# Performance work log

Hardware: AMD Instinct MI355X
Metric: run time of the kernel (lower is better)

## Reference

```python
import jax, jax.numpy as jnp
import numpy as np

B, D, H = 4096, 66, 512  # batch, system dim (22 atoms * 3), MLP hidden


def _dynamics(t, xs, W1, b1, W2, b2, W3, b3):
    # CNF vector field f(t, x): 3-layer SiLU MLP on concat([x, t])
    h = jnp.concatenate([xs, t], axis=1)          # [B, D+1]
    h = jax.nn.silu(h @ W1 + b1)                  # [B, H]
    h = jax.nn.silu(h @ W2 + b2)                  # [B, H]
    return h @ W3 + b3                            # [B, D]


def setup_inputs() -> dict:
    key = jax.random.key(0)
    ks = jax.random.split(key, 5)
    xs = jax.random.normal(ks[0], (B, D), dtype=jnp.float32)
    t = jax.random.uniform(ks[1], (B, 1), dtype=jnp.float32)
    W1 = jax.random.normal(ks[2], (D + 1, H), dtype=jnp.float32) / np.float32(np.sqrt(D + 1))
    b1 = jnp.zeros((H,), dtype=jnp.float32)
    W2 = jax.random.normal(ks[3], (H, H), dtype=jnp.float32) / np.float32(np.sqrt(H))
    b2 = jnp.zeros((H,), dtype=jnp.float32)
    W3 = jax.random.normal(ks[4], (H, D), dtype=jnp.float32) / np.float32(np.sqrt(H))
    b3 = jnp.zeros((D,), dtype=jnp.float32)
    return {"xs": xs, "t": t, "W1": W1, "b1": b1, "W2": W2, "b2": b2, "W3": W3, "b3": b3}


def reference(xs, t, W1, b1, W2, b2, W3, b3):
    # Exact divergence: trace of Jacobian d f / d x, computed with D JVPs
    # (forward-mode equivalent of the torch per-dim autograd.grad loop).
    def f(x):
        return _dynamics(t, x, W1, b1, W2, b2, W3, b3)

    dxs = f(xs)                                   # [B, D]
    eye = jnp.eye(D, dtype=xs.dtype)              # basis vectors e_i

    def jvp_col(e):
        _, tang = jax.jvp(f, (xs,), (jnp.broadcast_to(e, xs.shape),))
        return tang                               # J @ e_i, shape [B, D]

    tangs = jax.vmap(jvp_col)(eye)                # [D, B, D]
    div = jnp.einsum('dbd->b', tangs)             # sum_i (J e_i)_i = tr(J)
    return dxs, -div[:, None]
```

## Files before the change

### kernel.cpp

```cpp
#include <hip/hip_runtime.h>

#define Bn 4096
#define Dn 66
#define Hn 512

typedef __attribute__((ext_vector_type(8))) short short8;
typedef __attribute__((ext_vector_type(4))) float f32x4;

__device__ __forceinline__ unsigned short f2bf(float x) {
    union { float f; unsigned u; } v; v.f = x;
    unsigned r = v.u + 0x7fffu + ((v.u >> 16) & 1u);
    return (unsigned short)(r >> 16);
}
__device__ __forceinline__ float bf2f(unsigned short h) {
    union { float f; unsigned u; } v; v.u = ((unsigned)h) << 16; return v.f;
}


__global__ __launch_bounds__(512, 2) void k_pack(
    const float* __restrict__ W1, const float* __restrict__ W2,
    const float* __restrict__ W3,
    unsigned short* __restrict__ W2P, unsigned short* __restrict__ CmP,
    unsigned short* __restrict__ W3P)
{
    __shared__ float sW3[16*68];
    const int bid = blockIdx.x, tid = threadIdx.x;
    const int lane = tid & 63, wv = tid >> 6;

    if (bid < 64) {
        const int ct = bid >> 1;
        {
            const int r = tid >> 5, ii = tid & 31;
            const float* src = &W3[(size_t)(ct*16 + r)*Dn];
            sW3[r*68 + ii] = src[ii];
            sW3[r*68 + ii + 32] = src[ii + 32];
            if (ii < 2) sW3[r*68 + ii + 64] = src[ii + 64];
        }
        __syncthreads();
        const int ks = (bid & 1)*8 + wv;
        const int n = lane & 15, kg = lane >> 4;
        const int c = ct*16 + n;
        const int abase = ks*32 + kg*8;
        float w2v[8], m[8];
        #pragma unroll
        for (int j = 0; j < 8; ++j) {
            w2v[j] = W2[(size_t)(abase + j)*Hn + c];
            m[j] = 0.f;
        }
        #pragma unroll 2
        for (int i = 0; i < Dn; ++i) {
            const float w3 = sW3[n*68 + i];
            const float4 w1a = *(const float4*)&W1[(size_t)i*Hn + abase];
            const float4 w1b = *(const float4*)&W1[(size_t)i*Hn + abase + 4];
            m[0] = fmaf(w3, w1a.x, m[0]); m[1] = fmaf(w3, w1a.y, m[1]);
            m[2] = fmaf(w3, w1a.z, m[2]); m[3] = fmaf(w3, w1a.w, m[3]);
            m[4] = fmaf(w3, w1b.x, m[4]); m[5] = fmaf(w3, w1b.y, m[5]);
            m[6] = fmaf(w3, w1b.z, m[6]); m[7] = fmaf(w3, w1b.w, m[7]);
        }
        short8 pw, pc;
        #pragma unroll
        for (int j = 0; j < 8; ++j) {
            pw[j] = (short)f2bf(w2v[j]);
            pc[j] = (short)f2bf(w2v[j] * m[j]);
        }
        const size_t off = ((size_t)(ct*16 + ks)*64 + lane)*8;
        *(short8*)&W2P[off] = pw;
        *(short8*)&CmP[off] = pc;
    } else {
        const int tix = (bid - 64)*8 + wv;
        if (tix < 80) {
            const int ks = tix & 15;
            const int n = lane & 15, kg = lane >> 4;
            const int j_out = (tix >> 4)*16 + n;
            const int abase = ks*32 + kg*8;
            short8 p;
            #pragma unroll
            for (int j = 0; j < 8; ++j)
                p[j] = (j_out < Dn) ? (short)f2bf(W3[(size_t)(abase + j)*Dn + j_out]) : (short)0;
            *(short8*)&W3P[((size_t)tix*64 + lane)*8] = p;
        }
    }
}

__global__ __launch_bounds__(1024, 4) void k_main(
    const float* __restrict__ xs, const float* __restrict__ tt,
    const float* __restrict__ W1, const float* __restrict__ b1,
    const unsigned short* __restrict__ W2P, const unsigned short* __restrict__ CmP,
    const float* __restrict__ b2,
    const unsigned short* __restrict__ W3P, const float* __restrict__ b3,
    float* __restrict__ out)
{
    __shared__ __align__(16) unsigned short sA[3*8192];
    __shared__ float sX[67*16];
    __shared__ float sRed[16*16];

    const int tid = threadIdx.x, lane = tid & 63, wv = tid >> 6;
    const int rt = blockIdx.x, r0 = rt*16;
    const int n = lane & 15, kg = lane >> 4;
    const int rot = (blockIdx.x >> 3) & 15;

    for (int idx = tid; idx < 67*16; idx += 1024) {
        const int i = idx >> 4, r = idx & 15;
        sX[idx] = (i < Dn) ? xs[(size_t)(r0+r)*Dn + i] : tt[r0+r];
    }
    __syncthreads();

    {
        const int rg = lane & 7, cg = lane >> 3;
        const int c0 = wv*32 + cg*4;
        const int irot = (blockIdx.x >> 3) & 31;
        float z[2][4];
        {
            const float4 b4 = *(const float4*)&b1[c0];
            z[0][0]=b4.x; z[0][1]=b4.y; z[0][2]=b4.z; z[0][3]=b4.w;
            z[1][0]=b4.x; z[1][1]=b4.y; z[1][2]=b4.z; z[1][3]=b4.w;
        }
        #pragma unroll 2
        for (int s = 0; s < 67; ++s) {
            int i = s + irot; if (i >= 67) i -= 67;
            const float2 xf = *(const float2*)&sX[i*16 + 2*rg];
            const float4 wA = *(const float4*)&W1[(size_t)i*Hn + c0];
            const float ww[4] = {wA.x, wA.y, wA.z, wA.w};
            #pragma unroll
            for (int j = 0; j < 4; ++j) {
                z[0][j] = fmaf(xf.x, ww[j], z[0][j]);
                z[1][j] = fmaf(xf.y, ww[j], z[1][j]);
            }
        }
        const int kgrp = cg >> 1, joff = (cg & 1)*4;
        #pragma unroll
        for (int rr = 0; rr < 2; ++rr) {
            const int r = 2*rg + rr;
            ushort4 phi, plo, ps;
            unsigned short* PH = (unsigned short*)&phi;
            unsigned short* PL = (unsigned short*)&plo;
            unsigned short* PS = (unsigned short*)&ps;
            #pragma unroll
            for (int j = 0; j < 4; ++j) {
                const float zv = z[rr][j];
                const float sg = 1.f / (1.f + __expf(-zv));
                const float h  = zv * sg;
                const float sp = sg * (1.f + zv * (1.f - sg));
                const unsigned short hh = f2bf(h);
                PH[j] = hh;
                PL[j] = f2bf(h - bf2f(hh));
                PS[j] = f2bf(sp);
            }
            const int off = (wv*64 + r + 16*kgrp)*8 + joff;
            *(ushort4*)&sA[off]         = phi;
            *(ushort4*)&sA[8192 + off]  = plo;
            *(ushort4*)&sA[16384 + off] = ps;
        }
    }
    __syncthreads();

    const int ctb = wv*2;
    f32x4 zac[2], vac[2];
    #pragma unroll
    for (int ti = 0; ti < 2; ++ti) {
        const float bz = b2[(ctb + ti)*16 + n];
        zac[ti] = (f32x4){bz, bz, bz, bz};
        vac[ti] = (f32x4){0.f, 0.f, 0.f, 0.f};
    }
    #pragma unroll 2
    for (int s = 0; s < 16; ++s) {
        const int ks = (s + rot) & 15;
        const int ao = (ks*64 + lane)*8;
        const short8 ahi = *(const short8*)&sA[ao];
        const short8 alo = *(const short8*)&sA[8192 + ao];
        const short8 as1 = *(const short8*)&sA[16384 + ao];
        #pragma unroll
        for (int ti = 0; ti < 2; ++ti) {
            const size_t wo = ((size_t)((ctb + ti)*16 + ks)*64 + lane)*8;
            const short8 wf = *(const short8*)&W2P[wo];
            const short8 qf = *(const short8*)&CmP[wo];
            zac[ti] = __builtin_amdgcn_mfma_f32_16x16x32_bf16(ahi, wf, zac[ti], 0, 0, 0);
            zac[ti] = __builtin_amdgcn_mfma_f32_16x16x32_bf16(alo, wf, zac[ti], 0, 0, 0);
            vac[ti] = __builtin_amdgcn_mfma_f32_16x16x32_bf16(as1, qf, vac[ti], 0, 0, 0);
        }
    }
    __syncthreads();

    float dp[4] = {0.f, 0.f, 0.f, 0.f};
    #pragma unroll
    for (int ti = 0; ti < 2; ++ti) {
        const int c = (ctb + ti)*16 + n;
        const int ks2 = c >> 5, kg2 = (c >> 3) & 3, j2 = c & 7;
        #pragma unroll
        for (int q = 0; q < 4; ++q) {
            const float z2 = zac[ti][q];
            const float sg = 1.f / (1.f + __expf(-z2));
            const float h2 = z2 * sg;
            dp[q] = fmaf(sg * (1.f + z2 * (1.f - sg)), vac[ti][q], dp[q]);
            const unsigned short hh = f2bf(h2);
            const int o = (ks2*64 + (kg*4 + q) + 16*kg2)*8 + j2;
            sA[o] = hh;
            sA[8192 + o] = f2bf(h2 - bf2f(hh));
        }
    }
    #pragma unroll
    for (int q = 0; q < 4; ++q) {
        float v = dp[q];
        v += __shfl_xor(v, 1, 64);
        v += __shfl_xor(v, 2, 64);
        v += __shfl_xor(v, 4, 64);
        v += __shfl_xor(v, 8, 64);
        if (n == 0) sRed[wv*16 + kg*4 + q] = v;
    }
    __syncthreads();

    if (tid < 16) {
        float s = 0.f;
        #pragma unroll
        for (int q = 0; q < 16; ++q) s += sRed[q*16 + tid];
        out[(size_t)Bn*Dn + r0 + tid] = -s;
    }

    if (wv < 5) {
        const int jt = wv;
        const int j = jt*16 + n;
        const float bj = (j < Dn) ? b3[j] : 0.f;
        f32x4 oac = (f32x4){bj, bj, bj, bj};
        #pragma unroll 4
        for (int s = 0; s < 16; ++s) {
            const int ks = (s + rot) & 15;
            const int aoff = (ks*64 + lane)*8;
            const short8 ahi = *(const short8*)&sA[aoff];
            const short8 alo = *(const short8*)&sA[8192 + aoff];
            const short8 wf  = *(const short8*)&W3P[((size_t)(jt*16 + ks)*64 + lane)*8];
            oac = __builtin_amdgcn_mfma_f32_16x16x32_bf16(ahi, wf, oac, 0, 0, 0);
            oac = __builtin_amdgcn_mfma_f32_16x16x32_bf16(alo, wf, oac, 0, 0, 0);
        }
        if (j < Dn) {
            #pragma unroll
            for (int q = 0; q < 4; ++q)
                out[(size_t)(r0 + kg*4 + q)*Dn + j] = oac[q];
        }
    }
}

extern "C" void kernel_launch(void* const* d_in, const int* in_sizes, int n_in,
                              void* d_out, int out_size, void* d_ws, size_t ws_size,
                              hipStream_t stream)
{
    const float* xs = (const float*)d_in[0];
    const float* t  = (const float*)d_in[1];
    const float* W1 = (const float*)d_in[2];
    const float* b1 = (const float*)d_in[3];
    const float* W2 = (const float*)d_in[4];
    const float* b2 = (const float*)d_in[5];
    const float* W3 = (const float*)d_in[6];
    const float* b3 = (const float*)d_in[7];
    float* out = (float*)d_out;

    char* ws = (char*)d_ws;
    unsigned short* W2P = (unsigned short*)(ws);
    unsigned short* CmP = (unsigned short*)(ws + 524288);
    unsigned short* W3P = (unsigned short*)(ws + 1048576);

    k_pack<<<74,  512,  0, stream>>>(W1, W2, W3, W2P, CmP, W3P);
    k_main<<<256, 1024, 0, stream>>>(xs, t, W1, b1, W2P, CmP, b2, W3P, b3, out);
}
```

Measured before the change: 106.6 us.

## Split work per 32-row group across two blocks by hidden-column halves

```diff
diff --git a/kernel.cpp b/kernel.cpp
--- a/kernel.cpp
+++ b/kernel.cpp
@@ -15,7 +15,6 @@
 __device__ __forceinline__ float bf2f(unsigned short h) {
     union { float f; unsigned u; } v; v.u = ((unsigned)h) << 16; return v.f;
 }
-
 
 __global__ __launch_bounds__(512, 2) void k_pack(
     const float* __restrict__ W1, const float* __restrict__ W2,
@@ -88,19 +87,20 @@
     const unsigned short* __restrict__ W2P, const unsigned short* __restrict__ CmP,
     const float* __restrict__ b2,
     const unsigned short* __restrict__ W3P, const float* __restrict__ b3,
-    float* __restrict__ out)
-{
-    __shared__ __align__(16) unsigned short sA[3*8192];
-    __shared__ float sX[67*16];
-    __shared__ float sRed[16*16];
+    float* __restrict__ outP, float* __restrict__ dpP)
+{
+    __shared__ __align__(16) unsigned short sA[3*16384];
+    __shared__ float sX[67*32];
+    __shared__ float sRed[16*32];
 
     const int tid = threadIdx.x, lane = tid & 63, wv = tid >> 6;
-    const int rt = blockIdx.x, r0 = rt*16;
+    const int rg32 = blockIdx.x >> 1, half = blockIdx.x & 1;
+    const int r0 = rg32*32;
     const int n = lane & 15, kg = lane >> 4;
     const int rot = (blockIdx.x >> 3) & 15;
 
-    for (int idx = tid; idx < 67*16; idx += 1024) {
-        const int i = idx >> 4, r = idx & 15;
+    for (int idx = tid; idx < 67*32; idx += 1024) {
+        const int i = idx >> 5, r = idx & 31;
         sX[idx] = (i < Dn) ? xs[(size_t)(r0+r)*Dn + i] : tt[r0+r];
     }
     __syncthreads();
@@ -109,28 +109,32 @@
         const int rg = lane & 7, cg = lane >> 3;
         const int c0 = wv*32 + cg*4;
         const int irot = (blockIdx.x >> 3) & 31;
-        float z[2][4];
+        float z[4][4];
         {
             const float4 b4 = *(const float4*)&b1[c0];
-            z[0][0]=b4.x; z[0][1]=b4.y; z[0][2]=b4.z; z[0][3]=b4.w;
-            z[1][0]=b4.x; z[1][1]=b4.y; z[1][2]=b4.z; z[1][3]=b4.w;
+            #pragma unroll
+            for (int rr = 0; rr < 4; ++rr) { z[rr][0]=b4.x; z[rr][1]=b4.y; z[rr][2]=b4.z; z[rr][3]=b4.w; }
         }
         #pragma unroll 2
         for (int s = 0; s < 67; ++s) {
             int i = s + irot; if (i >= 67) i -= 67;
-            const float2 xf = *(const float2*)&sX[i*16 + 2*rg];
+            const float2 x0 = *(const float2*)&sX[i*32 + 2*rg];
+            const float2 x1 = *(const float2*)&sX[i*32 + 16 + 2*rg];
             const float4 wA = *(const float4*)&W1[(size_t)i*Hn + c0];
             const float ww[4] = {wA.x, wA.y, wA.z, wA.w};
             #pragma unroll
             for (int j = 0; j < 4; ++j) {
-                z[0][j] = fmaf(xf.x, ww[j], z[0][j]);
-                z[1][j] = fmaf(xf.y, ww[j], z[1][j]);
+                z[0][j] = fmaf(x0.x, ww[j], z[0][j]);
+                z[1][j] = fmaf(x0.y, ww[j], z[1][j]);
+                z[2][j] = fmaf(x1.x, ww[j], z[2][j]);
+                z[3][j] = fmaf(x1.y, ww[j], z[3][j]);
             }
         }
         const int kgrp = cg >> 1, joff = (cg & 1)*4;
         #pragma unroll
-        for (int rr = 0; rr < 2; ++rr) {
-            const int r = 2*rg + rr;
+        for (int rr = 0; rr < 4; ++rr) {
+            const int rtl = rr >> 1;
+            const int m = 2*(lane & 7) + (rr & 1);
             ushort4 phi, plo, ps;
             unsigned short* PH = (unsigned short*)&phi;
             unsigned short* PL = (unsigned short*)&plo;
@@ -146,96 +150,120 @@
                 PL[j] = f2bf(h - bf2f(hh));
                 PS[j] = f2bf(sp);
             }
-            const int off = (wv*64 + r + 16*kgrp)*8 + joff;
-            *(ushort4*)&sA[off]         = phi;
-            *(ushort4*)&sA[8192 + off]  = plo;
-            *(ushort4*)&sA[16384 + off] = ps;
-        }
-    }
-    __syncthreads();
-
-    const int ctb = wv*2;
+            const int off = ((rtl*16 + wv)*64 + m + 16*kgrp)*8 + joff;
+            *(ushort4*)&sA[off]          = phi;
+            *(ushort4*)&sA[16384 + off]  = plo;
+            *(ushort4*)&sA[32768 + off]  = ps;
+        }
+    }
+    __syncthreads();
+
+    const int ctb = half*16 + wv;
     f32x4 zac[2], vac[2];
-    #pragma unroll
-    for (int ti = 0; ti < 2; ++ti) {
-        const float bz = b2[(ctb + ti)*16 + n];
-        zac[ti] = (f32x4){bz, bz, bz, bz};
-        vac[ti] = (f32x4){0.f, 0.f, 0.f, 0.f};
+    {
+        const float bz = b2[ctb*16 + n];
+        zac[0] = (f32x4){bz, bz, bz, bz};
+        zac[1] = (f32x4){bz, bz, bz, bz};
+        vac[0] = (f32x4){0.f, 0.f, 0.f, 0.f};
+        vac[1] = (f32x4){0.f, 0.f, 0.f, 0.f};
     }
     #pragma unroll 2
     for (int s = 0; s < 16; ++s) {
         const int ks = (s + rot) & 15;
-        const int ao = (ks*64 + lane)*8;
-        const short8 ahi = *(const short8*)&sA[ao];
-        const short8 alo = *(const short8*)&sA[8192 + ao];
-        const short8 as1 = *(const short8*)&sA[16384 + ao];
-        #pragma unroll
-        for (int ti = 0; ti < 2; ++ti) {
-            const size_t wo = ((size_t)((ctb + ti)*16 + ks)*64 + lane)*8;
-            const short8 wf = *(const short8*)&W2P[wo];
-            const short8 qf = *(const short8*)&CmP[wo];
-            zac[ti] = __builtin_amdgcn_mfma_f32_16x16x32_bf16(ahi, wf, zac[ti], 0, 0, 0);
-            zac[ti] = __builtin_amdgcn_mfma_f32_16x16x32_bf16(alo, wf, zac[ti], 0, 0, 0);
-            vac[ti] = __builtin_amdgcn_mfma_f32_16x16x32_bf16(as1, qf, vac[ti], 0, 0, 0);
-        }
-    }
-    __syncthreads();
-
-    float dp[4] = {0.f, 0.f, 0.f, 0.f};
+        const size_t wo = ((size_t)(ctb*16 + ks)*64 + lane)*8;
+        const short8 wf = *(const short8*)&W2P[wo];
+        const short8 qf = *(const short8*)&CmP[wo];
+        #pragma unroll
+        for (int rtl = 0; rtl < 2; ++rtl) {
+            const int ao = ((rtl*16 + ks)*64 + lane)*8;
+            const short8 ahi = *(const short8*)&sA[ao];
+            const short8 alo = *(const short8*)&sA[16384 + ao];
+            const short8 as1 = *(const short8*)&sA[32768 + ao];
+            zac[rtl] = __builtin_amdgcn_mfma_f32_16x16x32_bf16(ahi, wf, zac[rtl], 0, 0, 0);
+            zac[rtl] = __builtin_amdgcn_mfma_f32_16x16x32_bf16(alo, wf, zac[rtl], 0, 0, 0);
+            vac[rtl] = __builtin_amdgcn_mfma_f32_16x16x32_bf16(as1, qf, vac[rtl], 0, 0, 0);
+        }
+    }
+    __syncthreads();
+
+    float dp[2][4] = {{0.f,0.f,0.f,0.f},{0.f,0.f,0.f,0.f}};
+    {
+        const int c_local = wv*16 + n;
+        const int ksl = c_local >> 5, kg2 = (c_local >> 3) & 3, j2 = c_local & 7;
+        #pragma unroll
+        for (int rtl = 0; rtl < 2; ++rtl) {
+            #pragma unroll
+            for (int q = 0; q < 4; ++q) {
+                const float z2 = zac[rtl][q];
+                const float sg = 1.f / (1.f + __expf(-z2));
+                const float h2 = z2 * sg;
+                dp[rtl][q] = fmaf(sg * (1.f + z2 * (1.f - sg)), vac[rtl][q], dp[rtl][q]);
+                const unsigned short hh = f2bf(h2);
+                const int o = ((rtl*8 + ksl)*64 + (kg*4 + q) + 16*kg2)*8 + j2;
+                sA[o] = hh;
+                sA[8192 + o] = f2bf(h2 - bf2f(hh));
+            }
+        }
+    }
     #pragma unroll
-    for (int ti = 0; ti < 2; ++ti) {
-        const int c = (ctb + ti)*16 + n;
-        const int ks2 = c >> 5, kg2 = (c >> 3) & 3, j2 = c & 7;
+    for (int rtl = 0; rtl < 2; ++rtl) {
         #pragma unroll
         for (int q = 0; q < 4; ++q) {
-            const float z2 = zac[ti][q];
-            const float sg = 1.f / (1.f + __expf(-z2));
-            const float h2 = z2 * sg;
-            dp[q] = fmaf(sg * (1.f + z2 * (1.f - sg)), vac[ti][q], dp[q]);
-            const unsigned short hh = f2bf(h2);
-            const int o = (ks2*64 + (kg*4 + q) + 16*kg2)*8 + j2;
-            sA[o] = hh;
-            sA[8192 + o] = f2bf(h2 - bf2f(hh));
-        }
-    }
-    #pragma unroll
-    for (int q = 0; q < 4; ++q) {
-        float v = dp[q];
-        v += __shfl_xor(v, 1, 64);
-        v += __shfl_xor(v, 2, 64);
-        v += __shfl_xor(v, 4, 64);
-        v += __shfl_xor(v, 8, 64);
-        if (n == 0) sRed[wv*16 + kg*4 + q] = v;
-    }
-    __syncthreads();
-
-    if (tid < 16) {
+            float v = dp[rtl][q];
+            v += __shfl_xor(v, 1, 64);
+            v += __shfl_xor(v, 2, 64);
+            v += __shfl_xor(v, 4, 64);
+            v += __shfl_xor(v, 8, 64);
+            if (n == 0) sRed[wv*32 + rtl*16 + kg*4 + q] = v;
+        }
+    }
+    __syncthreads();
+
+    if (tid < 32) {
         float s = 0.f;
         #pragma unroll
-        for (int q = 0; q < 16; ++q) s += sRed[q*16 + tid];
-        out[(size_t)Bn*Dn + r0 + tid] = -s;
-    }
-
-    if (wv < 5) {
-        const int jt = wv;
+        for (int q = 0; q < 16; ++q) s += sRed[q*32 + tid];
+        dpP[(size_t)half*Bn + r0 + tid] = s;
+    }
+
+    if (wv < 10) {
+        const int rtl = wv / 5, jt = wv % 5;
         const int j = jt*16 + n;
-        const float bj = (j < Dn) ? b3[j] : 0.f;
+        const float bj = (j < Dn && half == 0) ? b3[j] : 0.f;
         f32x4 oac = (f32x4){bj, bj, bj, bj};
         #pragma unroll 4
-        for (int s = 0; s < 16; ++s) {
-            const int ks = (s + rot) & 15;
-            const int aoff = (ks*64 + lane)*8;
-            const short8 ahi = *(const short8*)&sA[aoff];
-            const short8 alo = *(const short8*)&sA[8192 + aoff];
-            const short8 wf  = *(const short8*)&W3P[((size_t)(jt*16 + ks)*64 + lane)*8];
+        for (int s = 0; s < 8; ++s) {
+            const int ksl = (s + (rot & 7)) & 7;
+            const int ks_g = half*8 + ksl;
+            const int ao = ((rtl*8 + ksl)*64 + lane)*8;
+            const short8 ahi = *(const short8*)&sA[ao];
+            const short8 alo = *(const short8*)&sA[8192 + ao];
+            const short8 wf  = *(const short8*)&W3P[((size_t)(jt*16 + ks_g)*64 + lane)*8];
             oac = __builtin_amdgcn_mfma_f32_16x16x32_bf16(ahi, wf, oac, 0, 0, 0);
             oac = __builtin_amdgcn_mfma_f32_16x16x32_bf16(alo, wf, oac, 0, 0, 0);
         }
         if (j < Dn) {
             #pragma unroll
             for (int q = 0; q < 4; ++q)
-                out[(size_t)(r0 + kg*4 + q)*Dn + j] = oac[q];
-        }
+                outP[(size_t)half*Bn*Dn + (size_t)(r0 + rtl*16 + kg*4 + q)*Dn + j] = oac[q];
+        }
+    }
+}
+
+__global__ __launch_bounds__(256) void k_final(
+    const float* __restrict__ outP, const float* __restrict__ dpP,
+    float* __restrict__ out)
+{
+    const int bid = blockIdx.x, tid = threadIdx.x;
+    if (bid < 264) {
+        const size_t t = (size_t)bid*256 + tid;
+        const float4 a = ((const float4*)outP)[t];
+        const float4 b = ((const float4*)(outP + (size_t)Bn*Dn))[t];
+        float4 r; r.x = a.x+b.x; r.y = a.y+b.y; r.z = a.z+b.z; r.w = a.w+b.w;
+        ((float4*)out)[t] = r;
+    } else {
+        const int r = (bid - 264)*256 + tid;
+        out[(size_t)Bn*Dn + r] = -(dpP[r] + dpP[Bn + r]);
     }
 }
 
@@ -257,7 +285,10 @@
     unsigned short* W2P = (unsigned short*)(ws);
     unsigned short* CmP = (unsigned short*)(ws + 524288);
     unsigned short* W3P = (unsigned short*)(ws + 1048576);
-
-    k_pack<<<74,  512,  0, stream>>>(W1, W2, W3, W2P, CmP, W3P);
-    k_main<<<256, 1024, 0, stream>>>(xs, t, W1, b1, W2P, CmP, b2, W3P, b3, out);
-}
+    float*         outP = (float*)(ws + 1130496);
+    float*          dpP = (float*)(ws + 1130496 + 2*(size_t)Bn*Dn*4);
+
+    k_pack <<<74,  512,  0, stream>>>(W1, W2, W3, W2P, CmP, W3P);
+    k_main <<<256, 1024, 0, stream>>>(xs, t, W1, b1, W2P, CmP, b2, W3P, b3, outP, dpP);
+    k_final<<<280, 256,  0, stream>>>(outP, dpP, out);
+}
```

Result: slower. 109.7 us (+3.0%).
